# Kernel tuning notes

Hardware: AMD Instinct MI355X
Metric: run time of the kernel (lower is better)

The kernel has to match this reference:

```python
import jax, jax.numpy as jnp
import numpy as np

L = 4          # GAT_LAYERS
HEADS = 4      # N_HEADS
H = 64         # transformer hidden dim
DH = H // HEADS
FIN = 32       # NODE_EMBED_SIZE
A = 15         # gats.num_actions (readout size)
OBS = 1500     # flattened obs dim
HS = 512       # hidden_size (policy FC)
NOUT = 15      # num_outputs
VH = 128       # VALUE_HIDDENS
B = 128        # batch of graphs
N = 1000       # nodes per map graph
TOT = B * N
DEG = 4
E = TOT * DEG


def _lin(key, fan_in, shape):
    return jax.random.normal(key, shape, jnp.float32) * (1.0 / np.sqrt(fan_in))


def setup_inputs() -> dict:
    key = jax.random.key(0)
    ks = jax.random.split(key, 30)
    node_feats = jax.random.normal(ks[0], (TOT, FIN), jnp.float32)
    obs = jax.random.normal(ks[1], (B, OBS), jnp.float32)
    # batched-graph edges: endpoints stay within each graph (DGL batch semantics)
    off = (jnp.arange(B) * N)[:, None]
    edge_src = (jax.random.randint(ks[2], (B, N * DEG), 0, N) + off).reshape(-1).astype(jnp.int32)
    edge_dst = (jax.random.randint(ks[3], (B, N * DEG), 0, N) + off).reshape(-1).astype(jnp.int32)
    agent_nodes = (jax.random.randint(ks[4], (B,), 0, N) + jnp.arange(B) * N).astype(jnp.int32)
    p = {
        'W_in': _lin(ks[5], FIN, (FIN, H)),
        'Wq': _lin(ks[6], H, (L, H, H)), 'Wk': _lin(ks[7], H, (L, H, H)),
        'Wv': _lin(ks[8], H, (L, H, H)), 'Wo': _lin(ks[9], H, (L, H, H)),
        'ln1_g': jnp.ones((L, H), jnp.float32), 'ln1_b': jnp.zeros((L, H), jnp.float32),
        'W1': _lin(ks[10], H, (L, H, 2 * H)), 'b1': jnp.zeros((L, 2 * H), jnp.float32),
        'W2': _lin(ks[11], 2 * H, (L, 2 * H, H)), 'b2': jnp.zeros((L, H), jnp.float32),
        'ln2_g': jnp.ones((L, H), jnp.float32), 'ln2_b': jnp.zeros((L, H), jnp.float32),
        'Wr': _lin(ks[12], H, (H, A)), 'br': jnp.zeros((A,), jnp.float32),
        'Wp1': _lin(ks[13], A + OBS, (A + OBS, HS)), 'bp1': jnp.zeros((HS,), jnp.float32),
        'Wp2': _lin(ks[14], HS, (HS, HS)), 'bp2': jnp.zeros((HS,), jnp.float32),
        'Wlog': _lin(ks[15], HS, (HS, NOUT)), 'blog': jnp.zeros((NOUT,), jnp.float32),
        'Wv1': _lin(ks[16], OBS, (OBS, VH)), 'bv1': jnp.zeros((VH,), jnp.float32),
        'Wv2': _lin(ks[17], VH, (VH, VH)), 'bv2': jnp.zeros((VH,), jnp.float32),
        'Wvo': _lin(ks[18], VH, (VH, 1)), 'bvo': jnp.zeros((1,), jnp.float32),
    }
    return dict(node_feats=node_feats, obs=obs, edge_src=edge_src, edge_dst=edge_dst,
                agent_nodes=agent_nodes, **p)


def _layernorm(x, g, b):
    m = x.mean(-1, keepdims=True)
    v = ((x - m) ** 2).mean(-1, keepdims=True)
    return (x - m) * jax.lax.rsqrt(v + 1e-5) * g + b


def reference(node_feats, obs, edge_src, edge_dst, agent_nodes, W_in, Wq, Wk, Wv, Wo,
              ln1_g, ln1_b, W1, b1, W2, b2, ln2_g, ln2_b, Wr, br,
              Wp1, bp1, Wp2, bp2, Wlog, blog, Wv1, bv1, Wv2, bv2, Wvo, bvo):
    n = node_feats.shape[0]
    x = node_feats @ W_in                                   # [n, H]
    inv_sqrt_dh = np.float32(1.0 / np.sqrt(DH))
    for l in range(L):
        q = (x @ Wq[l]).reshape(n, HEADS, DH)
        k = (x @ Wk[l]).reshape(n, HEADS, DH)
        v = (x @ Wv[l]).reshape(n, HEADS, DH)
        # per-edge attention scores, softmax over incoming edges of each dst node
        s = jnp.sum(q[edge_dst] * k[edge_src], axis=-1) * inv_sqrt_dh   # [E, HEADS]
        m = jax.ops.segment_max(s, edge_dst, num_segments=n)            # [n, HEADS]
        w = jnp.exp(s - m[edge_dst])
        denom = jax.ops.segment_sum(w, edge_dst, num_segments=n)        # [n, HEADS]
        agg = jax.ops.segment_sum(w[:, :, None] * v[edge_src], edge_dst, num_segments=n)
        attn = (agg / (denom[:, :, None] + 1e-9)).reshape(n, H) @ Wo[l]
        x = _layernorm(x + attn, ln1_g[l], ln1_b[l])
        h = jax.nn.relu(x @ W1[l] + b1[l]) @ W2[l] + b2[l]
        x = _layernorm(x + h, ln2_g[l], ln2_b[l])
    gat_out = x[agent_nodes] @ Wr + br                      # [B, A] per-agent action features
    feat = jnp.tanh(jnp.concatenate([gat_out, obs], axis=1) @ Wp1 + bp1)
    feat = jnp.tanh(feat @ Wp2 + bp2)
    logits = feat @ Wlog + blog                             # [B, NOUT]
    vh = jnp.tanh(obs @ Wv1 + bv1)
    vh = jnp.tanh(vh @ Wv2 + bv2)
    value = (vh @ Wvo + bvo)[:, 0]                          # [B]
    return logits, value
```

## Files before the change

kernel.cpp:

```cpp
#include <hip/hip_runtime.h>
#include <hip/hip_bf16.h>
#include <cstdint>
#include <cstddef>

#define DEV static __device__ __forceinline__

constexpr int GRAPHS = 128;
constexpr int NPG    = 1000;
constexpr int EPG    = 4000;
constexpr int TOTN   = GRAPHS * NPG;
constexpr int TOTE   = GRAPHS * EPG;
constexpr int HD     = 64;
constexpr int OBSD   = 1500;
constexpr int AD     = 15;

typedef __attribute__((ext_vector_type(8))) short bf16x8;
typedef __attribute__((ext_vector_type(4))) float f32x4;

DEV unsigned short f2b(float f){
  unsigned u = __float_as_uint(f);
  return (unsigned short)((u + 0x7fffu + ((u >> 16) & 1u)) >> 16);
}
DEV float b2f(unsigned short s){ return __uint_as_float((unsigned)s << 16); }

DEV void fma4(float4& a, float s, const float4 w){
  a.x = fmaf(s, w.x, a.x); a.y = fmaf(s, w.y, a.y);
  a.z = fmaf(s, w.z, a.z); a.w = fmaf(s, w.w, a.w);
}

DEV ushort4 pack4(float4 v){
  ushort4 r; r.x=f2b(v.x); r.y=f2b(v.y); r.z=f2b(v.z); r.w=f2b(v.w); return r;
}

__global__ __launch_bounds__(256) void k_wprep(const float* __restrict__ Wq,
    const float* __restrict__ Wk, const float* __restrict__ Wv,
    const float* __restrict__ Wo, const float* __restrict__ W1,
    const float* __restrict__ W2, unsigned short* __restrict__ wpack){
  int e = blockIdx.x*256 + threadIdx.x;
  int l = e >> 15;
  int r = e & 32767;
  float val;
  if (r < 12288){
    int c = r >> 6, k = r & 63;
    val = (c < 64)  ? Wq[l*4096 + k*64 + c]
        : (c < 128) ? Wk[l*4096 + k*64 + (c-64)]
                    : Wv[l*4096 + k*64 + (c-128)];
  } else if (r < 16384){
    int i = r - 12288; int c = i >> 6, k = i & 63;
    val = Wo[l*4096 + k*64 + c];
  } else if (r < 24576){
    int i = r - 16384; int c = i >> 6, k = i & 63;
    val = W1[l*8192 + k*128 + c];
  } else {
    int i = r - 24576; int c = i >> 7, k = i & 127;
    val = W2[l*8192 + k*64 + c];
  }
  wpack[e] = f2b(val);
}

__global__ __launch_bounds__(256) void k_zero(int* __restrict__ cnt){
  cnt[blockIdx.x*256 + threadIdx.x] = 0;
}

__global__ __launch_bounds__(256) void k_hist(const int* __restrict__ edst,
                                              int* __restrict__ cnt){
  int e = blockIdx.x*256 + threadIdx.x;
  atomicAdd(&cnt[edst[e]], 1);
}

__global__ __launch_bounds__(1024) void k_scan(const int* __restrict__ cnt,
    int* __restrict__ rstart, int* __restrict__ cursor){
  __shared__ int s[1024];
  const int g = blockIdx.x, tid = threadIdx.x;
  int v = (tid < NPG) ? cnt[g*NPG + tid] : 0;
  s[tid] = v;
  __syncthreads();
  #pragma unroll
  for (int off=1; off<1024; off<<=1){
    int t = (tid >= off) ? s[tid-off] : 0;
    __syncthreads();
    s[tid] += t;
    __syncthreads();
  }
  if (tid < NPG){
    int r = g*EPG + (s[tid] - v);
    rstart[g*NPG+tid] = r;
    cursor[g*NPG+tid] = r;
  }
}

__global__ __launch_bounds__(256) void k_scatter(const int* __restrict__ esrc,
    const int* __restrict__ edst, int* __restrict__ cursor,
    int* __restrict__ esorted){
  int e = blockIdx.x*256 + threadIdx.x;
  int pos = atomicAdd(&cursor[edst[e]], 1);
  esorted[pos] = esrc[e];
}

__global__ __launch_bounds__(256) void k_in(const float* __restrict__ nf,
                                            const float* __restrict__ Win,
                                            unsigned short* __restrict__ xb){
  __shared__ float  s_nf[256*36];
  __shared__ float4 s_w[512];
  const int tid = threadIdx.x;
  const int node0 = blockIdx.x * 256;
  const float4* W4 = (const float4*)Win;
  s_w[tid] = W4[tid]; s_w[tid+256] = W4[tid+256];
  const float4* nf4 = (const float4*)nf;
  float4* snf4 = (float4*)s_nf;
  #pragma unroll
  for (int r=0;r<8;r++){
    int i = tid + 256*r; int n = i>>3, k4 = i&7;
    snf4[n*9 + k4] = nf4[(size_t)(node0+n)*8 + k4];
  }
  __syncthreads();
  const int ng = tid>>2, cg = tid&3;
  float4 acc[4][4];
  #pragma unroll
  for (int i=0;i<4;i++){ acc[i][0]=make_float4(0,0,0,0); acc[i][1]=make_float4(0,0,0,0);
                         acc[i][2]=make_float4(0,0,0,0); acc[i][3]=make_float4(0,0,0,0); }
  #pragma unroll 4
  for (int k=0;k<32;k++){
    float nv[4];
    #pragma unroll
    for (int i=0;i<4;i++) nv[i] = s_nf[(ng + 64*i)*36 + k];
    float4 w[4];
    #pragma unroll
    for (int j=0;j<4;j++) w[j] = s_w[k*16 + cg*4 + j];
    #pragma unroll
    for (int i=0;i<4;i++){
      #pragma unroll
      for (int j=0;j<4;j++) fma4(acc[i][j], nv[i], w[j]);
    }
  }
  ushort4* xb4 = (ushort4*)xb;
  #pragma unroll
  for (int i=0;i<4;i++){
    size_t nidx = (size_t)(node0 + ng + 64*i) * 16;
    #pragma unroll
    for (int j=0;j<4;j++) xb4[nidx + cg*4 + j] = pack4(acc[i][j]);
  }
}

__global__ __launch_bounds__(256) void k_qkv_m(const unsigned short* __restrict__ xb,
    const unsigned short* __restrict__ wqkvT,
    unsigned short* __restrict__ qkv){
  __shared__ short s_w[192*72];
  __shared__ short s_st[4][16*104];
  const int tid = threadIdx.x;
  const int node0 = blockIdx.x * 256;
  {
    const unsigned* src = (const unsigned*)wqkvT;
    unsigned* dst = (unsigned*)s_w;
    #pragma unroll
    for (int r=0;r<24;r++){
      int j = tid + 256*r;
      int c = j >> 5, kk = j & 31;
      dst[c*36 + kk] = src[j];
    }
  }
  __syncthreads();
  const int lane = tid & 63, wave = tid >> 6;
  const int m = lane & 15, quad = lane >> 4;
  const int rowbase = node0 + wave*64;
  bf16x8 af[4][2];
  #pragma unroll
  for (int rt=0;rt<4;rt++){
    const unsigned short* xp = xb + (size_t)(rowbase + rt*16 + m)*64 + quad*8;
    af[rt][0] = *(const bf16x8*)xp;
    af[rt][1] = *(const bf16x8*)(xp + 32);
  }
  short* st = s_st[wave];
  #pragma unroll
  for (int rt=0;rt<4;rt++){
    #pragma unroll
    for (int half=0; half<2; half++){
      #pragma unroll
      for (int c6=0;c6<6;c6++){
        int ct = half*6 + c6;
        bf16x8 b0 = *(const bf16x8*)&s_w[(ct*16+m)*72 + quad*8];
        bf16x8 b1 = *(const bf16x8*)&s_w[(ct*16+m)*72 + 32 + quad*8];
        f32x4 acc = {0.f,0.f,0.f,0.f};
        acc = __builtin_amdgcn_mfma_f32_16x16x32_bf16(af[rt][0], b0, acc, 0,0,0);
        acc = __builtin_amdgcn_mfma_f32_16x16x32_bf16(af[rt][1], b1, acc, 0,0,0);
        #pragma unroll
        for (int i=0;i<4;i++)
          st[(quad*4+i)*104 + c6*16 + m] = (short)f2b(acc[i]);
      }
      #pragma unroll
      for (int j=0;j<3;j++){
        int flat = (j*64 + lane)*8;
        int r = flat / 96, c = flat % 96;
        bf16x8 v = *(const bf16x8*)&st[r*104 + c];
        *(bf16x8*)(qkv + (size_t)(rowbase + rt*16 + r)*192 + half*96 + c) = v;
      }
    }
  }
}

__global__ __launch_bounds__(256) void k_edge2(const unsigned short* __restrict__ qkv,
    const int* __restrict__ rstart, const int* __restrict__ cnt,
    const int* __restrict__ esorted, unsigned short* __restrict__ attn_in){
  const int tid = threadIdx.x;
  const int wb = (blockIdx.x & 7)*1000 + (blockIdx.x >> 3);
  const int lane = tid & 63;
  const int sub  = lane >> 4;
  const int dg   = lane & 15;
  const int wave = tid >> 6;
  const int node = wb*16 + wave*4 + sub;
  const ushort4* row = (const ushort4*)(qkv + (size_t)node*192);
  ushort4 qu = row[dg];
  float q0 = b2f(qu.x), q1 = b2f(qu.y), q2 = b2f(qu.z), q3 = b2f(qu.w);
  const int rs = rstart[node];
  const int n  = cnt[node];
  float a0=0.f, a1=0.f, a2=0.f, a3=0.f, den=0.f;
  int src = (n > 0) ? esorted[rs] : 0;
  ushort4 ku = *(const ushort4*)(qkv + (size_t)src*192 + 64 + dg*4);
  ushort4 vu = *(const ushort4*)(qkv + (size_t)src*192 + 128 + dg*4);
  for (int i=0;i<n;i++){
    ushort4 cku = ku, cvu = vu;
    if (i+1 < n){
      int s2 = esorted[rs + i + 1];
      ku = *(const ushort4*)(qkv + (size_t)s2*192 + 64 + dg*4);
      vu = *(const ushort4*)(qkv + (size_t)s2*192 + 128 + dg*4);
    }
    float p = q0*b2f(cku.x) + q1*b2f(cku.y) + q2*b2f(cku.z) + q3*b2f(cku.w);
    p += __shfl_xor(p, 1);
    p += __shfl_xor(p, 2);
    float w = __expf(p * 0.25f);
    den += w;
    a0 = fmaf(w, b2f(cvu.x), a0);
    a1 = fmaf(w, b2f(cvu.y), a1);
    a2 = fmaf(w, b2f(cvu.z), a2);
    a3 = fmaf(w, b2f(cvu.w), a3);
  }
  float inv = 1.0f/(den + 1e-9f);
  ushort4 o;
  o.x = f2b(a0*inv); o.y = f2b(a1*inv); o.z = f2b(a2*inv); o.w = f2b(a3*inv);
  ((ushort4*)attn_in)[(size_t)node*16 + dg] = o;
}

__global__ __launch_bounds__(256) void k_attn_ffn(
    const unsigned short* __restrict__ attn_in,
    unsigned short* __restrict__ xb,
    const unsigned short* __restrict__ woT,
    const unsigned short* __restrict__ w1T, const float* __restrict__ b1_l,
    const unsigned short* __restrict__ w2T, const float* __restrict__ b2_l,
    const float* __restrict__ l1g, const float* __restrict__ l1b,
    const float* __restrict__ l2g, const float* __restrict__ l2b){
  __shared__ short s_w1[128*72];
  __shared__ short s_w2[64*136];
  __shared__ short s_st[4][16*136];
  const int tid = threadIdx.x;
  const int node0 = blockIdx.x*256;
  {
    const unsigned* src = (const unsigned*)w1T;
    unsigned* dst = (unsigned*)s_w1;
    #pragma unroll
    for (int r=0;r<16;r++){
      int j = tid + 256*r;
      int c = j >> 5, kk = j & 31;
      dst[c*36 + kk] = src[j];
    }
  }
  {
    const unsigned* src = (const unsigned*)w2T;
    unsigned* dst = (unsigned*)s_w2;
    #pragma unroll
    for (int r=0;r<16;r++){
      int j = tid + 256*r;
      int c = j >> 6, kk = j & 63;
      dst[c*68 + kk] = src[j];
    }
  }
  const int lane = tid&63, wave = tid>>6;
  const int m = lane&15, quad = lane>>4;
  const int rowbase = node0 + wave*64;
  bf16x8 wo[4][2];
  #pragma unroll
  for (int ct=0;ct<4;ct++){
    wo[ct][0] = *(const bf16x8*)&woT[(ct*16+m)*64 + quad*8];
    wo[ct][1] = *(const bf16x8*)&woT[(ct*16+m)*64 + 32 + quad*8];
  }
  float g1[4], bb1[4], g2[4], bb2[4], b2v[4];
  #pragma unroll
  for (int ct=0;ct<4;ct++){
    g1[ct]=l1g[ct*16+m]; bb1[ct]=l1b[ct*16+m];
    g2[ct]=l2g[ct*16+m]; bb2[ct]=l2b[ct*16+m];
    b2v[ct]=b2_l[ct*16+m];
  }
  float b1v[8];
  #pragma unroll
  for (int ct=0;ct<8;ct++) b1v[ct]=b1_l[ct*16+m];
  bf16x8 af[4][2];
  #pragma unroll
  for (int rt=0;rt<4;rt++){
    const unsigned short* ap = attn_in + (size_t)(rowbase + rt*16 + m)*64 + quad*8;
    af[rt][0] = *(const bf16x8*)ap;
    af[rt][1] = *(const bf16x8*)(ap + 32);
  }
  __syncthreads();
  short* st = s_st[wave];
  #pragma unroll
  for (int rt=0;rt<4;rt++){
    f32x4 acc[4];
    #pragma unroll
    for (int ct=0;ct<4;ct++){
      f32x4 z = {0.f,0.f,0.f,0.f};
      z = __builtin_amdgcn_mfma_f32_16x16x32_bf16(af[rt][0], wo[ct][0], z, 0,0,0);
      z = __builtin_amdgcn_mfma_f32_16x16x32_bf16(af[rt][1], wo[ct][1], z, 0,0,0);
      acc[ct] = z;
    }
    float x1v[4][4];
    #pragma unroll
    for (int i=0;i<4;i++){
      size_t row = (size_t)(rowbase + rt*16 + quad*4 + i)*64;
      float v0 = acc[0][i] + b2f(xb[row + m]);
      float v1 = acc[1][i] + b2f(xb[row + 16 + m]);
      float v2 = acc[2][i] + b2f(xb[row + 32 + m]);
      float v3 = acc[3][i] + b2f(xb[row + 48 + m]);
      float sm = v0+v1+v2+v3;
      float sq = v0*v0+v1*v1+v2*v2+v3*v3;
      #pragma unroll
      for (int mk=1; mk<16; mk<<=1){ sm += __shfl_xor(sm, mk); sq += __shfl_xor(sq, mk); }
      float mean = sm*0.015625f;
      float var  = sq*0.015625f - mean*mean;
      float rs   = rsqrtf(var + 1e-5f);
      x1v[i][0] = (v0-mean)*rs*g1[0]+bb1[0];
      x1v[i][1] = (v1-mean)*rs*g1[1]+bb1[1];
      x1v[i][2] = (v2-mean)*rs*g1[2]+bb1[2];
      x1v[i][3] = (v3-mean)*rs*g1[3]+bb1[3];
      int rl = quad*4 + i;
      st[rl*136 + m]      = (short)f2b(x1v[i][0]);
      st[rl*136 + 16 + m] = (short)f2b(x1v[i][1]);
      st[rl*136 + 32 + m] = (short)f2b(x1v[i][2]);
      st[rl*136 + 48 + m] = (short)f2b(x1v[i][3]);
    }
    bf16x8 x10 = *(const bf16x8*)&st[m*136 + quad*8];
    bf16x8 x11 = *(const bf16x8*)&st[m*136 + 32 + quad*8];
    #pragma unroll
    for (int ct=0;ct<8;ct++){
      bf16x8 b0 = *(const bf16x8*)&s_w1[(ct*16+m)*72 + quad*8];
      bf16x8 b1 = *(const bf16x8*)&s_w1[(ct*16+m)*72 + 32 + quad*8];
      f32x4 z = {0.f,0.f,0.f,0.f};
      z = __builtin_amdgcn_mfma_f32_16x16x32_bf16(x10, b0, z, 0,0,0);
      z = __builtin_amdgcn_mfma_f32_16x16x32_bf16(x11, b1, z, 0,0,0);
      #pragma unroll
      for (int i=0;i<4;i++)
        st[(quad*4+i)*136 + ct*16 + m] = (short)f2b(fmaxf(z[i]+b1v[ct], 0.f));
    }
    bf16x8 h0 = *(const bf16x8*)&st[m*136 + quad*8];
    bf16x8 h1 = *(const bf16x8*)&st[m*136 + 32 + quad*8];
    bf16x8 h2 = *(const bf16x8*)&st[m*136 + 64 + quad*8];
    bf16x8 h3 = *(const bf16x8*)&st[m*136 + 96 + quad*8];
    f32x4 acc2[4];
    #pragma unroll
    for (int ct=0;ct<4;ct++){
      f32x4 z = {0.f,0.f,0.f,0.f};
      z = __builtin_amdgcn_mfma_f32_16x16x32_bf16(h0, *(const bf16x8*)&s_w2[(ct*16+m)*136 + quad*8],      z, 0,0,0);
      z = __builtin_amdgcn_mfma_f32_16x16x32_bf16(h1, *(const bf16x8*)&s_w2[(ct*16+m)*136 + 32 + quad*8], z, 0,0,0);
      z = __builtin_amdgcn_mfma_f32_16x16x32_bf16(h2, *(const bf16x8*)&s_w2[(ct*16+m)*136 + 64 + quad*8], z, 0,0,0);
      z = __builtin_amdgcn_mfma_f32_16x16x32_bf16(h3, *(const bf16x8*)&s_w2[(ct*16+m)*136 + 96 + quad*8], z, 0,0,0);
      acc2[ct] = z;
    }
    #pragma unroll
    for (int i=0;i<4;i++){
      float v0 = acc2[0][i] + b2v[0] + x1v[i][0];
      float v1 = acc2[1][i] + b2v[1] + x1v[i][1];
      float v2 = acc2[2][i] + b2v[2] + x1v[i][2];
      float v3 = acc2[3][i] + b2v[3] + x1v[i][3];
      float sm = v0+v1+v2+v3;
      float sq = v0*v0+v1*v1+v2*v2+v3*v3;
      #pragma unroll
      for (int mk=1; mk<16; mk<<=1){ sm += __shfl_xor(sm, mk); sq += __shfl_xor(sq, mk); }
      float mean = sm*0.015625f;
      float var  = sq*0.015625f - mean*mean;
      float rs   = rsqrtf(var + 1e-5f);
      int rl = quad*4 + i;
      st[rl*136 + m]      = (short)f2b((v0-mean)*rs*g2[0]+bb2[0]);
      st[rl*136 + 16 + m] = (short)f2b((v1-mean)*rs*g2[1]+bb2[1]);
      st[rl*136 + 32 + m] = (short)f2b((v2-mean)*rs*g2[2]+bb2[2]);
      st[rl*136 + 48 + m] = (short)f2b((v3-mean)*rs*g2[3]+bb2[3]);
    }
    #pragma unroll
    for (int j=0;j<2;j++){
      int flat = (j*64 + lane)*8;
      int r = flat >> 6, c = flat & 63;
      bf16x8 v = *(const bf16x8*)&st[r*136 + c];
      *(bf16x8*)(xb + (size_t)(rowbase + rt*16 + r)*64 + c) = v;
    }
  }
}

__global__ __launch_bounds__(512) void k_fc1(const unsigned short* __restrict__ xb,
    const float* __restrict__ obs, const int* __restrict__ agents,
    const float* __restrict__ Wr, const float* __restrict__ br,
    const float* __restrict__ Wp1, float* __restrict__ part1){
  constexpr int ROWS=2, COLS=256, CH=384, K=1515, N=512;
  const int chunk = 379;
  __shared__ float s_a[ROWS*CH];
  const int tid = threadIdx.x;
  const int ct = blockIdx.x, rg = blockIdx.y, ks = blockIdx.z;
  const int k0 = ks * chunk;
  const int len = min(K - k0, chunk);
  const int row0 = rg * ROWS;
  #pragma unroll
  for (int rr=0; rr<ROWS; rr++)
    for (int i=tid; i<len; i+=512){
      int k = k0 + i;
      if (k >= AD) s_a[rr*CH + i] = obs[(size_t)(row0+rr)*OBSD + (k-AD)];
    }
  if (ks==0 && tid < ROWS*AD){
    int rr = tid/AD, c = tid%AD;
    int b = row0 + rr;
    const unsigned short* xa = xb + (size_t)agents[b]*HD;
    float a = br[c];
    #pragma unroll 8
    for (int k=0;k<HD;k++) a = fmaf(b2f(xa[k]), Wr[k*AD + c], a);
    s_a[rr*CH + c] = a;
  }
  __syncthreads();
  const int r = tid / COLS, c = tid % COLS;
  const float* wp = Wp1 + (size_t)k0*N + ct*COLS + c;
  const float* ap = s_a + r*CH;
  float acc = 0.f;
  #pragma unroll 8
  for (int k=0;k<len;k++) acc = fmaf(ap[k], wp[(size_t)k*N], acc);
  part1[((size_t)ks*128 + row0 + r)*N + ct*COLS + c] = acc;
}

__global__ __launch_bounds__(512) void k_fc2(const float* __restrict__ part1,
    const float* __restrict__ bp1, const float* __restrict__ Wp2,
    float* __restrict__ part2){
  constexpr int ROWS=2, COLS=256, CH=256, N=512;
  __shared__ float s_a[ROWS*CH];
  const int tid = threadIdx.x;
  const int ct = blockIdx.x, rg = blockIdx.y, ks = blockIdx.z;
  const int k0 = ks * CH;
  const int row0 = rg * ROWS;
  #pragma unroll
  for (int rr=0; rr<ROWS; rr++)
    for (int i=tid; i<CH; i+=512){
      int k = k0 + i;
      float s = bp1[k];
      #pragma unroll
      for (int j=0;j<4;j++) s += part1[((size_t)j*128 + row0+rr)*512 + k];
      s_a[rr*CH + i] = tanhf(s);
    }
  __syncthreads();
  const int r = tid / COLS, c = tid % COLS;
  const float* wp = Wp2 + (size_t)k0*N + ct*COLS + c;
  const float* ap = s_a + r*CH;
  float acc = 0.f;
  #pragma unroll 8
  for (int k=0;k<CH;k++) acc = fmaf(ap[k], wp[(size_t)k*N], acc);
  part2[((size_t)ks*128 + row0 + r)*N + ct*COLS + c] = acc;
}

__global__ __launch_bounds__(256) void k_logits(const float* __restrict__ part2,
    const float* __restrict__ bp2, const float* __restrict__ Wlog,
    const float* __restrict__ blog, float* __restrict__ out){
  __shared__ float s_f[512];
  __shared__ float s_p[16*AD];
  const int b = blockIdx.x, tid = threadIdx.x;
  for (int i=tid;i<512;i+=256){
    float s = bp2[i] + part2[(size_t)b*512 + i] + part2[(size_t)(128+b)*512 + i];
    s_f[i] = tanhf(s);
  }
  __syncthreads();
  if (tid < 240){
    int c = tid % AD, kc = tid / AD;
    float a = 0.f;
    #pragma unroll 8
    for (int j=0;j<32;j++){ int k = kc*32 + j; a = fmaf(s_f[k], Wlog[k*AD + c], a); }
    s_p[tid] = a;
  }
  __syncthreads();
  if (tid < AD){
    float a = blog[tid];
    #pragma unroll
    for (int kc=0;kc<16;kc++) a += s_p[kc*AD + tid];
    out[(size_t)b*AD + tid] = a;
  }
}

template<int ROWS, int COLS, int CH, int KS, int N>
__global__ __launch_bounds__(ROWS*COLS) void k_gemm_part(
    const float* __restrict__ A, int lda, int K,
    const float* __restrict__ W, float* __restrict__ part){
  constexpr int BT = ROWS*COLS;
  __shared__ float s_a[ROWS*CH];
  const int tid = threadIdx.x;
  const int ct = blockIdx.x, rg = blockIdx.y, ks = blockIdx.z;
  const int chunk = (K + KS - 1) / KS;
  const int k0 = ks * chunk;
  const int len = min(K - k0, chunk);
  const int row0 = rg * ROWS;
  #pragma unroll
  for (int rr=0; rr<ROWS; rr++)
    for (int i=tid; i<len; i+=BT)
      s_a[rr*CH + i] = A[(size_t)(row0+rr)*lda + k0 + i];
  __syncthreads();
  const int r = tid / COLS, c = tid % COLS;
  const float* wp = W + (size_t)k0*N + ct*COLS + c;
  const float* ap = s_a + r*CH;
  float acc = 0.f;
  #pragma unroll 8
  for (int k=0;k<len;k++) acc = fmaf(ap[k], wp[(size_t)k*N], acc);
  part[((size_t)ks*128 + row0 + r)*N + ct*COLS + c] = acc;
}

__global__ __launch_bounds__(128) void k_vfin(const float* __restrict__ partv,
    const float* __restrict__ bv1, const float* __restrict__ Wv2,
    const float* __restrict__ bv2, const float* __restrict__ Wvo,
    const float* __restrict__ bvo, float* __restrict__ out){
  __shared__ float s_v[128];
  __shared__ float s_r[128];
  const int b = blockIdx.x, tid = threadIdx.x;
  {
    float s = bv1[tid];
    #pragma unroll
    for (int j=0;j<8;j++) s += partv[((size_t)j*128 + b)*128 + tid];
    s_v[tid] = tanhf(s);
  }
  __syncthreads();
  float a = bv2[tid];
  #pragma unroll 8
  for (int k=0;k<128;k++) a = fmaf(s_v[k], Wv2[k*128 + tid], a);
  s_r[tid] = tanhf(a) * Wvo[tid];
  __syncthreads();
  if (tid < 64){
    float v = s_r[tid] + s_r[tid+64];
    #pragma unroll
    for (int m=32;m>=1;m>>=1) v += __shfl_xor(v, m);
    if (tid==0) out[GRAPHS*AD + b] = v + bvo[0];
  }
}

extern "C" void kernel_launch(void* const* d_in, const int* in_sizes, int n_in,
                              void* d_out, int out_size, void* d_ws, size_t ws_size,
                              hipStream_t stream) {
  (void)in_sizes; (void)n_in; (void)out_size; (void)ws_size;
  const float* nf     = (const float*)d_in[0];
  const float* obs    = (const float*)d_in[1];
  const int*   esrc   = (const int*)d_in[2];
  const int*   edst   = (const int*)d_in[3];
  const int*   agents = (const int*)d_in[4];
  const float* Win    = (const float*)d_in[5];
  const float* Wq     = (const float*)d_in[6];
  const float* Wk     = (const float*)d_in[7];
  const float* Wv     = (const float*)d_in[8];
  const float* Wo     = (const float*)d_in[9];
  const float* ln1g   = (const float*)d_in[10];
  const float* ln1b   = (const float*)d_in[11];
  const float* W1     = (const float*)d_in[12];
  const float* b1     = (const float*)d_in[13];
  const float* W2     = (const float*)d_in[14];
  const float* b2     = (const float*)d_in[15];
  const float* ln2g   = (const float*)d_in[16];
  const float* ln2b   = (const float*)d_in[17];
  const float* Wr     = (const float*)d_in[18];
  const float* br     = (const float*)d_in[19];
  const float* Wp1    = (const float*)d_in[20];
  const float* bp1    = (const float*)d_in[21];
  const float* Wp2    = (const float*)d_in[22];
  const float* bp2    = (const float*)d_in[23];
  const float* Wlog   = (const float*)d_in[24];
  const float* blog   = (const float*)d_in[25];
  const float* Wv1    = (const float*)d_in[26];
  const float* bv1    = (const float*)d_in[27];
  const float* Wv2    = (const float*)d_in[28];
  const float* bv2    = (const float*)d_in[29];
  const float* Wvo    = (const float*)d_in[30];
  const float* bvo    = (const float*)d_in[31];
  float* out = (float*)d_out;

  unsigned short* xb      = (unsigned short*)d_ws;
  unsigned short* qkv     = xb + (size_t)TOTN*HD;
  unsigned short* attn_in = qkv + (size_t)TOTN*192;
  unsigned short* wpack   = attn_in + (size_t)TOTN*HD;
  int* cnt     = (int*)(wpack + 131072);
  int* rstart  = cnt + TOTN;
  int* cursor  = rstart + TOTN;
  int* esorted = cursor + TOTN;
  float* part1 = (float*)(esorted + TOTE);
  float* part2 = part1 + 4*128*512;
  float* partv = part2 + 2*128*512;

  k_wprep  <<<512, 256, 0, stream>>>(Wq, Wk, Wv, Wo, W1, W2, wpack);
  k_zero   <<<TOTN/256, 256, 0, stream>>>(cnt);
  k_hist   <<<TOTE/256, 256, 0, stream>>>(edst, cnt);
  k_scan   <<<GRAPHS, 1024, 0, stream>>>(cnt, rstart, cursor);
  k_scatter<<<TOTE/256, 256, 0, stream>>>(esrc, edst, cursor, esorted);

  k_in<<<TOTN/256, 256, 0, stream>>>(nf, Win, xb);
  for (int l=0; l<4; l++){
    const unsigned short* wl = wpack + l*32768;
    k_qkv_m   <<<TOTN/256, 256, 0, stream>>>(xb, wl, qkv);
    k_edge2   <<<TOTN/16, 256, 0, stream>>>(qkv, rstart, cnt, esorted, attn_in);
    k_attn_ffn<<<TOTN/256, 256, 0, stream>>>(attn_in, xb,
                                             wl + 12288,
                                             wl + 16384, b1 + l*128,
                                             wl + 24576, b2 + l*64,
                                             ln1g + l*64, ln1b + l*64,
                                             ln2g + l*64, ln2b + l*64);
  }
  k_fc1   <<<dim3(2,64,4), 512, 0, stream>>>(xb, obs, agents, Wr, br, Wp1, part1);
  k_fc2   <<<dim3(2,64,2), 512, 0, stream>>>(part1, bp1, Wp2, part2);
  k_logits<<<GRAPHS, 256, 0, stream>>>(part2, bp2, Wlog, blog, out);
  k_gemm_part<4,128,192,8,128><<<dim3(1,32,8), 512, 0, stream>>>(obs, 1500, 1500, Wv1, partv);
  k_vfin  <<<GRAPHS, 128, 0, stream>>>(partv, bv1, Wv2, bv2, Wvo, bvo, out);
}
```

Baseline: 510.4 us.

## Assign one wave per node and split incoming edges across quarter-waves

The edge-attention kernel now gives each destination node a whole wave instead of a 16-lane group. The four 16-lane quarters each take every fourth incoming edge, and the partial softmax sums and weighted values are combined with cross-lane shuffles at the end. This aims to cut the serial per-node loop length and expose more gather parallelism for the in-degree-imbalanced edges. In exchange it launches four times as many blocks, drops the software prefetch, and does extra shuffle reductions plus masked dummy loads.

```diff
diff --git a/kernel.cpp b/kernel.cpp
--- a/kernel.cpp
+++ b/kernel.cpp
@@ -198,46 +198,46 @@
   }
 }
 
-__global__ __launch_bounds__(256) void k_edge2(const unsigned short* __restrict__ qkv,
+__global__ __launch_bounds__(256) void k_edge3(const unsigned short* __restrict__ qkv,
     const int* __restrict__ rstart, const int* __restrict__ cnt,
     const int* __restrict__ esorted, unsigned short* __restrict__ attn_in){
-  const int tid = threadIdx.x;
-  const int wb = (blockIdx.x & 7)*1000 + (blockIdx.x >> 3);
-  const int lane = tid & 63;
-  const int sub  = lane >> 4;
-  const int dg   = lane & 15;
-  const int wave = tid >> 6;
-  const int node = wb*16 + wave*4 + sub;
-  const ushort4* row = (const ushort4*)(qkv + (size_t)node*192);
-  ushort4 qu = row[dg];
+  const int tid  = threadIdx.x;
+  const int wave = tid >> 6, lane = tid & 63;
+  const int quad = lane >> 4, dg = lane & 15;
+  const int unit = (blockIdx.x & 7)*4000 + (blockIdx.x >> 3);
+  const int node = unit*4 + wave;
+  ushort4 qu = *(const ushort4*)(qkv + (size_t)node*192 + dg*4);
   float q0 = b2f(qu.x), q1 = b2f(qu.y), q2 = b2f(qu.z), q3 = b2f(qu.w);
   const int rs = rstart[node];
   const int n  = cnt[node];
   float a0=0.f, a1=0.f, a2=0.f, a3=0.f, den=0.f;
-  int src = (n > 0) ? esorted[rs] : 0;
-  ushort4 ku = *(const ushort4*)(qkv + (size_t)src*192 + 64 + dg*4);
-  ushort4 vu = *(const ushort4*)(qkv + (size_t)src*192 + 128 + dg*4);
-  for (int i=0;i<n;i++){
-    ushort4 cku = ku, cvu = vu;
-    if (i+1 < n){
-      int s2 = esorted[rs + i + 1];
-      ku = *(const ushort4*)(qkv + (size_t)s2*192 + 64 + dg*4);
-      vu = *(const ushort4*)(qkv + (size_t)s2*192 + 128 + dg*4);
-    }
-    float p = q0*b2f(cku.x) + q1*b2f(cku.y) + q2*b2f(cku.z) + q3*b2f(cku.w);
+  for (int j=0; j*4 < n; j++){
+    int i = j*4 + quad;
+    bool valid = (i < n);
+    int src = valid ? esorted[rs + i] : node;
+    ushort4 ku = *(const ushort4*)(qkv + (size_t)src*192 + 64 + dg*4);
+    ushort4 vu = *(const ushort4*)(qkv + (size_t)src*192 + 128 + dg*4);
+    float p = q0*b2f(ku.x) + q1*b2f(ku.y) + q2*b2f(ku.z) + q3*b2f(ku.w);
     p += __shfl_xor(p, 1);
     p += __shfl_xor(p, 2);
-    float w = __expf(p * 0.25f);
+    float w = valid ? __expf(p * 0.25f) : 0.f;
     den += w;
-    a0 = fmaf(w, b2f(cvu.x), a0);
-    a1 = fmaf(w, b2f(cvu.y), a1);
-    a2 = fmaf(w, b2f(cvu.z), a2);
-    a3 = fmaf(w, b2f(cvu.w), a3);
-  }
-  float inv = 1.0f/(den + 1e-9f);
-  ushort4 o;
-  o.x = f2b(a0*inv); o.y = f2b(a1*inv); o.z = f2b(a2*inv); o.w = f2b(a3*inv);
-  ((ushort4*)attn_in)[(size_t)node*16 + dg] = o;
+    a0 = fmaf(w, b2f(vu.x), a0);
+    a1 = fmaf(w, b2f(vu.y), a1);
+    a2 = fmaf(w, b2f(vu.z), a2);
+    a3 = fmaf(w, b2f(vu.w), a3);
+  }
+  den += __shfl_xor(den, 16); den += __shfl_xor(den, 32);
+  a0  += __shfl_xor(a0, 16);  a0  += __shfl_xor(a0, 32);
+  a1  += __shfl_xor(a1, 16);  a1  += __shfl_xor(a1, 32);
+  a2  += __shfl_xor(a2, 16);  a2  += __shfl_xor(a2, 32);
+  a3  += __shfl_xor(a3, 16);  a3  += __shfl_xor(a3, 32);
+  if (quad == 0){
+    float inv = 1.0f/(den + 1e-9f);
+    ushort4 o;
+    o.x = f2b(a0*inv); o.y = f2b(a1*inv); o.z = f2b(a2*inv); o.w = f2b(a3*inv);
+    ((ushort4*)attn_in)[(size_t)node*16 + dg] = o;
+  }
 }
 
 __global__ __launch_bounds__(256) void k_attn_ffn(
@@ -597,7 +597,7 @@
   for (int l=0; l<4; l++){
     const unsigned short* wl = wpack + l*32768;
     k_qkv_m   <<<TOTN/256, 256, 0, stream>>>(xb, wl, qkv);
-    k_edge2   <<<TOTN/16, 256, 0, stream>>>(qkv, rstart, cnt, esorted, attn_in);
+    k_edge3   <<<TOTN/4, 256, 0, stream>>>(qkv, rstart, cnt, esorted, attn_in);
     k_attn_ffn<<<TOTN/256, 256, 0, stream>>>(attn_in, xb,
                                              wl + 12288,
                                              wl + 16384, b1 + l*128,
```

Result: slower. 562.1 us (+10.1%).
